# Kernel tuning notes

Measured on AMD Instinct MI355X. Metric: run time of the kernel, lower is better.

Reference implementation:

```python
import jax, jax.numpy as jnp
import numpy as np

B = 262144
STATE_DIM = 12
ACTION_DIM = 1
MSG_DIM = 32
MAX_CHILDREN = 2
EPS = 1e-12  # F.normalize default eps


def _l2norm(x):
    n = jnp.sqrt(jnp.sum(x * x, axis=-1, keepdims=True))
    return x / jnp.maximum(n, EPS)


def setup_inputs() -> dict:
    key = jax.random.key(0)
    ks = jax.random.split(key, 16)

    def lin(kw, kb, out_d, in_d):
        lim = 1.0 / np.sqrt(in_d)
        w = jax.random.uniform(kw, (out_d, in_d), jnp.float32, -lim, lim)
        b = jax.random.uniform(kb, (out_d,), jnp.float32, -lim, lim)
        return w, b

    state = jax.random.normal(ks[0], (B, STATE_DIM), jnp.float32)
    action = jax.random.normal(ks[1], (B, ACTION_DIM), jnp.float32)

    # ModelUp (sNet): fc1, fc2, fc3
    up_w1, up_b1 = lin(ks[2], ks[3], 64, STATE_DIM + ACTION_DIM)
    up_w2, up_b2 = lin(ks[4], ks[5], 64, 64 + MSG_DIM * MAX_CHILDREN)
    up_w3, up_b3 = lin(ks[6], ks[7], MSG_DIM, 64)

    # ModelDownAction.model = MLPBase(msg_dim + action_dim + msg_dim, msg_dim)
    dyn_w1, dyn_b1 = lin(ks[8], ks[9], 400, MSG_DIM + ACTION_DIM + MSG_DIM)
    dyn_w2, dyn_b2 = lin(ks[10], ks[11], 300, 400)
    dyn_w3, dyn_b3 = lin(ks[12], ks[13], MSG_DIM, 300)

    return dict(state=state, action=action,
                up_w1=up_w1, up_b1=up_b1, up_w2=up_w2, up_b2=up_b2,
                up_w3=up_w3, up_b3=up_b3,
                dyn_w1=dyn_w1, dyn_b1=dyn_b1, dyn_w2=dyn_w2, dyn_b2=dyn_b2,
                dyn_w3=dyn_w3, dyn_b3=dyn_b3)


def reference(state, action,
              up_w1, up_b1, up_w2, up_b2, up_w3, up_b3,
              dyn_w1, dyn_b1, dyn_w2, dyn_b2, dyn_w3, dyn_b3):
    # num_limbs == 1, parents = [-1], td = bu = True, disable_fold = True
    x = state                              # (B, state_dim)
    u = action                             # (B, 1)

    # ---- bottom_up_transmission(0): ModelUp with all-zero child messages ----
    m_children = jnp.zeros((B, MSG_DIM * MAX_CHILDREN), x.dtype)
    xu = jnp.concatenate([x, u], axis=-1)
    xu = _l2norm(xu @ up_w1.T + up_b1)                       # (B, 64)
    xum = jnp.tanh(jnp.concatenate([xu, m_children], axis=-1))
    xum = jnp.tanh(xum @ up_w2.T + up_b2)                    # (B, 64)
    msg_up = _l2norm(xum @ up_w3.T + up_b3)                  # (B, msg_dim)

    # ---- top_down_transmission(0): ModelDownAction, state := msg_up ----
    # parent_msg = zeros, self_children_idx = 0 -> msg_in = zeros slice
    msg_in = jnp.zeros((B, MSG_DIM), x.dtype)
    xum2 = jnp.concatenate([msg_up, u, msg_in], axis=-1)     # (B, 2*msg_dim+1)
    h = jax.nn.relu(xum2 @ dyn_w1.T + dyn_b1)                # (B, 400)
    h = jax.nn.relu(h @ dyn_w2.T + dyn_b2)                   # (B, 300)
    delta = h @ dyn_w3.T + dyn_b3                            # (B, msg_dim)

    # stack over num_limbs=1 then squeeze -> (B, msg_dim)
    return delta
```

## Files before the change

### kernel.cpp

```cpp
#include <hip/hip_runtime.h>
#include <stdint.h>

typedef short s16x8 __attribute__((ext_vector_type(8)));
typedef float f32x16 __attribute__((ext_vector_type(16)));
typedef unsigned int u32;
typedef unsigned int u32x2 __attribute__((ext_vector_type(2)));

#define NFRAG 336
#define WS_USHORTS (NFRAG*512)
#define PANEL_BYTES 16384
#define LDS_BYTES (2*PANEL_BYTES)

#define MFMA(a,b,c) __builtin_amdgcn_mfma_f32_32x32x16_bf16((a),(b),(c),0,0,0)

__device__ __forceinline__ unsigned short f2bf(float f){
  u32 x = __builtin_bit_cast(u32, f);
  x += 0x7fffu + ((x >> 16) & 1u);
  return (unsigned short)(x >> 16);
}

__device__ __forceinline__ float bfhi(float b){
  return __builtin_bit_cast(float, (u32)f2bf(b) << 16);
}

__device__ __forceinline__ u32 pkbf(float a, float b){
  u32 r;
  asm("v_cvt_pk_bf16_f32 %0, %1, %2" : "=v"(r) : "v"(a), "v"(b));
  return r;
}

__device__ __forceinline__ float fast_tanh(float x){
  float ax = fabsf(x);
  float e = __expf(-2.0f * ax);
  float r = (1.0f - e) * __builtin_amdgcn_rcpf(1.0f + e);
  return x < 0.0f ? -r : r;
}

__device__ __forceinline__ float halfsum(float s){
  return s + __shfl_xor(s, 32);
}

__device__ __forceinline__ void tile2frags(const f32x16 v, s16x8& f0, s16x8& f1){
  u32 w00 = pkbf(v[0],  v[1]),  w01 = pkbf(v[2],  v[3]);
  u32 w10 = pkbf(v[4],  v[5]),  w11 = pkbf(v[6],  v[7]);
  u32 w20 = pkbf(v[8],  v[9]),  w21 = pkbf(v[10], v[11]);
  u32 w30 = pkbf(v[12], v[13]), w31 = pkbf(v[14], v[15]);
  u32x2 p0 = __builtin_amdgcn_permlane32_swap(w00, w10, false, false);
  u32x2 p1 = __builtin_amdgcn_permlane32_swap(w01, w11, false, false);
  u32x2 p2 = __builtin_amdgcn_permlane32_swap(w20, w30, false, false);
  u32x2 p3 = __builtin_amdgcn_permlane32_swap(w21, w31, false, false);
  int4 r0, r1;
  r0.x = (int)p0[0]; r0.y = (int)p1[0]; r0.z = (int)p0[1]; r0.w = (int)p1[1];
  r1.x = (int)p2[0]; r1.y = (int)p3[0]; r1.z = (int)p2[1]; r1.w = (int)p3[1];
  f0 = __builtin_bit_cast(s16x8, r0);
  f1 = __builtin_bit_cast(s16x8, r1);
}

__global__ void wconv_kernel(const float* __restrict__ uw1, const float* __restrict__ ub1,
                             const float* __restrict__ uw2, const float* __restrict__ ub2,
                             const float* __restrict__ uw3, const float* __restrict__ ub3,
                             const float* __restrict__ dw1, const float* __restrict__ db1,
                             const float* __restrict__ dw2, const float* __restrict__ db2,
                             const float* __restrict__ dw3, const float* __restrict__ db3,
                             unsigned short* __restrict__ wp)
{
  int i = blockIdx.x*256 + threadIdx.x;
  if (i >= WS_USHORTS) return;
  int f    = i >> 9;
  int lane = (i >> 3) & 63;
  int j    = i & 7;
  int row  = lane & 31;
  int k8   = (lane >> 5)*8 + j;
  float v = 0.0f;
  if (f < 2){
    int feat = f*32 + row; int k = k8;
    if (k < 13) v = uw1[feat*13 + k];
    else if (k == 13) v = ub1[feat];
    else if (k == 14) v = ub1[feat] - bfhi(ub1[feat]);
  } else if (f < 12){
    int t = f - 2; int kt = t >> 1, nt = t & 1;
    int feat = nt*32 + row; int k = kt*16 + k8;
    if (k < 64) v = uw2[feat*128 + k];
    else if (k == 64) v = ub2[feat];
    else if (k == 65) v = ub2[feat] - bfhi(ub2[feat]);
  } else if (f < 17){
    int kt = f - 12; int feat = row; int k = kt*16 + k8;
    if (k < 64) v = uw3[feat*64 + k];
    else if (k == 64) v = ub3[feat];
    else if (k == 65) v = ub3[feat] - bfhi(ub3[feat]);
  } else if (f < 56){
    int t = f - 17; int nt = t/3, kt = t%3;
    int feat = nt*32 + row; int k = kt*16 + k8;
    if (feat < 400){
      if (k < 33) v = dw1[feat*65 + k];
      else if (k == 33) v = db1[feat];
      else if (k == 34) v = db1[feat] - bfhi(db1[feat]);
    } else if ((feat == 400 || feat == 401) && k == 33) v = 1.0f;
  } else {
    int t = f - 56; int n = t/56; int r = t%56;
    if (r < 52){
      int kf = r >> 1, nt = r & 1;
      int feat = n*64 + nt*32 + row; int k = kf*16 + k8;
      if (feat < 300){
        if (k < 400) v = dw2[feat*400 + k];
        else if (k == 400) v = db2[feat];
        else if (k == 401) v = db2[feat] - bfhi(db2[feat]);
      } else if ((feat == 300 || feat == 301) && k == 400) v = 1.0f;
    } else {
      int kt = n*4 + (r - 52); int feat = row; int k = kt*16 + k8;
      if (k < 300) v = dw3[feat*300 + k];
      else if (k == 300) v = db3[feat];
      else if (k == 301) v = db3[feat] - bfhi(db3[feat]);
    }
  }
  wp[i] = f2bf(v);
}

__device__ __forceinline__ s16x8 fragF(const char* sm, int f, int ln){
  return *(const s16x8*)(sm + ((f >> 4) & 1)*PANEL_BYTES + (f & 15)*1024 + ln*16);
}

__device__ __forceinline__ void stage16(const unsigned short* wp, char* sm, int panel, int tid){
  char* dst = sm + (panel & 1)*PANEL_BYTES;
  const char* src = (const char*)wp + (size_t)panel*PANEL_BYTES;
  #pragma unroll
  for (int j = 0; j < 8; ++j){
    int off = j*2048 + tid*16;
    __builtin_amdgcn_global_load_lds(
      (const __attribute__((address_space(1))) unsigned int*)(src + off),
      (__attribute__((address_space(3))) unsigned int*)(dst + off), 16, 0, 0);
  }
}

#define BND(P) { __syncthreads(); if ((P) <= 20) stage16(wp, sm, (P), tid); }

#define D1TRIPLE(f0_, oA, oB) { \
  f32x16 a = {}; \
  __builtin_amdgcn_s_setprio(1); \
  a = MFMA(fragF(sm, (f0_)+0, ln), mf0, a); \
  a = MFMA(fragF(sm, (f0_)+1, ln), mf1, a); \
  a = MFMA(fragF(sm, (f0_)+2, ln), mf2, a); \
  __builtin_amdgcn_s_setprio(0); \
  _Pragma("unroll") \
  for (int r = 0; r < 16; ++r) a[r] = fmaxf(a[r], 0.f); \
  tile2frags(a, oA, oB); }

#define D2RUN(fb, r0, r1) { \
  __builtin_amdgcn_s_setprio(1); \
  _Pragma("unroll") \
  for (int r = (r0); r < (r1); ++r){ \
    s16x8 hb = h1f[r>>1]; \
    if (r & 1) d2a1 = MFMA(fragF(sm, (fb)+r, ln), hb, d2a1); \
    else       d2a0 = MFMA(fragF(sm, (fb)+r, ln), hb, d2a0); \
  } \
  __builtin_amdgcn_s_setprio(0); }

#define D2TAIL(fb) { \
  _Pragma("unroll") \
  for (int r = 0; r < 16; ++r){ \
    d2a0[r] = fmaxf(d2a0[r], 0.f); \
    d2a1[r] = fmaxf(d2a1[r], 0.f); \
  } \
  s16x8 c0, c1, c2, c3; \
  tile2frags(d2a0, c0, c1); \
  tile2frags(d2a1, c2, c3); \
  __builtin_amdgcn_s_setprio(1); \
  acc3 = MFMA(fragF(sm, (fb)+52, ln), c0, acc3); \
  acc3 = MFMA(fragF(sm, (fb)+53, ln), c1, acc3); \
  acc3 = MFMA(fragF(sm, (fb)+54, ln), c2, acc3); \
  acc3 = MFMA(fragF(sm, (fb)+55, ln), c3, acc3); \
  __builtin_amdgcn_s_setprio(0); }

__global__ __launch_bounds__(128, 2) void fused_kernel(
    const float* __restrict__ state, const float* __restrict__ action,
    const unsigned short* __restrict__ wp, float* __restrict__ out)
{
  __shared__ __align__(1024) char sm[LDS_BYTES];

  const int tid = threadIdx.x;
  const int ln  = tid & 63;
  const int wid = tid >> 6;
  const int c   = ln & 31;
  const int h   = ln >> 5;
  const int rowb = blockIdx.x*64 + wid*32;

  const float* xr = state + (size_t)(rowb + c)*12;
  float u = action[rowb + c];
  float4 xa, xb;
  if (h == 0){
    xa = *(const float4*)xr;
    xb = *(const float4*)(xr + 4);
  } else {
    xa = *(const float4*)(xr + 8);
    xb = float4{u, 1.0f, 1.0f, 0.0f};
  }

  stage16(wp, sm, 0, tid);
  BND(1)

  int4 xw;
  xw.x = pkbf(xa.x, xa.y); xw.y = pkbf(xa.z, xa.w);
  xw.z = pkbf(xb.x, xb.y); xw.w = pkbf(xb.z, xb.w);
  s16x8 xfrag = __builtin_bit_cast(s16x8, xw);
  int4 ow = {0,0,0,0}; if (h == 0) ow.x = 0x3F803F80;
  s16x8 onef = __builtin_bit_cast(s16x8, ow);
  int4 mw = {0,0,0,0};
  if (h == 0){ mw.x = pkbf(u, 1.0f); mw.y = 0x3F80; }
  s16x8 mf2 = __builtin_bit_cast(s16x8, mw);

  s16x8 mf0, mf1;
  {
    s16x8 xf0, xf1, xf2, xf3, tf0, tf1, tf2, tf3;
    {
      f32x16 a0 = {}, a1 = {};
      a0 = MFMA(fragF(sm, 0, ln), xfrag, a0);
      a1 = MFMA(fragF(sm, 1, ln), xfrag, a1);
      float s = 0.f;
      #pragma unroll
      for (int r = 0; r < 16; ++r) s += a0[r]*a0[r] + a1[r]*a1[r];
      s = halfsum(s);
      float inv = __builtin_amdgcn_rsqf(fmaxf(s, 1e-24f));
      #pragma unroll
      for (int r = 0; r < 16; ++r){
        a0[r] = fast_tanh(a0[r]*inv);
        a1[r] = fast_tanh(a1[r]*inv);
      }
      tile2frags(a0, xf0, xf1);
      tile2frags(a1, xf2, xf3);
    }
    {
      f32x16 a0 = {}, a1 = {};
      __builtin_amdgcn_s_setprio(1);
      a0 = MFMA(fragF(sm, 2, ln), xf0, a0);  a1 = MFMA(fragF(sm, 3, ln), xf0, a1);
      a0 = MFMA(fragF(sm, 4, ln), xf1, a0);  a1 = MFMA(fragF(sm, 5, ln), xf1, a1);
      a0 = MFMA(fragF(sm, 6, ln), xf2, a0);  a1 = MFMA(fragF(sm, 7, ln), xf2, a1);
      a0 = MFMA(fragF(sm, 8, ln), xf3, a0);  a1 = MFMA(fragF(sm, 9, ln), xf3, a1);
      a0 = MFMA(fragF(sm,10, ln), onef, a0); a1 = MFMA(fragF(sm,11, ln), onef, a1);
      __builtin_amdgcn_s_setprio(0);
      #pragma unroll
      for (int r = 0; r < 16; ++r){
        a0[r] = fast_tanh(a0[r]);
        a1[r] = fast_tanh(a1[r]);
      }
      tile2frags(a0, tf0, tf1);
      tile2frags(a1, tf2, tf3);
    }
    {
      f32x16 m = {};
      __builtin_amdgcn_s_setprio(1);
      m = MFMA(fragF(sm,12, ln), tf0, m);
      m = MFMA(fragF(sm,13, ln), tf1, m);
      m = MFMA(fragF(sm,14, ln), tf2, m);
      m = MFMA(fragF(sm,15, ln), tf3, m);
      __builtin_amdgcn_s_setprio(0);
      BND(2)
      __builtin_amdgcn_s_setprio(1);
      m = MFMA(fragF(sm,16, ln), onef, m);
      __builtin_amdgcn_s_setprio(0);
      float s = 0.f;
      #pragma unroll
      for (int r = 0; r < 16; ++r) s += m[r]*m[r];
      s = halfsum(s);
      float inv = __builtin_amdgcn_rsqf(fmaxf(s, 1e-24f));
      #pragma unroll
      for (int r = 0; r < 16; ++r) m[r] *= inv;
      tile2frags(m, mf0, mf1);
    }
  }

  s16x8 h1f[26];
  D1TRIPLE(17, h1f[0],  h1f[1])
  D1TRIPLE(20, h1f[2],  h1f[3])
  D1TRIPLE(23, h1f[4],  h1f[5])
  D1TRIPLE(26, h1f[6],  h1f[7])
  D1TRIPLE(29, h1f[8],  h1f[9])
  BND(3)
  D1TRIPLE(32, h1f[10], h1f[11])
  D1TRIPLE(35, h1f[12], h1f[13])
  D1TRIPLE(38, h1f[14], h1f[15])
  D1TRIPLE(41, h1f[16], h1f[17])
  D1TRIPLE(44, h1f[18], h1f[19])
  {
    f32x16 a = {};
    __builtin_amdgcn_s_setprio(1);
    a = MFMA(fragF(sm, 47, ln), mf0, a);
    __builtin_amdgcn_s_setprio(0);
    BND(4)
    __builtin_amdgcn_s_setprio(1);
    a = MFMA(fragF(sm, 48, ln), mf1, a);
    a = MFMA(fragF(sm, 49, ln), mf2, a);
    __builtin_amdgcn_s_setprio(0);
    #pragma unroll
    for (int r = 0; r < 16; ++r) a[r] = fmaxf(a[r], 0.f);
    tile2frags(a, h1f[20], h1f[21]);
  }
  D1TRIPLE(50, h1f[22], h1f[23])
  D1TRIPLE(53, h1f[24], h1f[25])

  f32x16 acc3 = {};
  {
    f32x16 d2a0 = {}, d2a1 = {};
    D2RUN(56, 0, 8)
    BND(5)
    D2RUN(56, 8, 24)
    BND(6)
    D2RUN(56, 24, 40)
    BND(7)
    D2RUN(56, 40, 52)
    D2TAIL(56)
  }
  {
    f32x16 d2a0 = {}, d2a1 = {};
    BND(8)
    D2RUN(112, 0, 16)
    BND(9)
    D2RUN(112, 16, 32)
    BND(10)
    D2RUN(112, 32, 48)
    BND(11)
    D2RUN(112, 48, 52)
    D2TAIL(112)
  }
  {
    f32x16 d2a0 = {}, d2a1 = {};
    D2RUN(168, 0, 8)
    BND(12)
    D2RUN(168, 8, 24)
    BND(13)
    D2RUN(168, 24, 40)
    BND(14)
    D2RUN(168, 40, 52)
    D2TAIL(168)
  }
  {
    f32x16 d2a0 = {}, d2a1 = {};
    BND(15)
    D2RUN(224, 0, 16)
    BND(16)
    D2RUN(224, 16, 32)
    BND(17)
    D2RUN(224, 32, 48)
    BND(18)
    D2RUN(224, 48, 52)
    D2TAIL(224)
  }
  {
    f32x16 d2a0 = {}, d2a1 = {};
    D2RUN(280, 0, 8)
    BND(19)
    D2RUN(280, 8, 24)
    BND(20)
    D2RUN(280, 24, 40)
    BND(21)
    D2RUN(280, 40, 52)
    D2TAIL(280)
  }

  float* op = out + (size_t)(rowb + c)*32;
  #pragma unroll
  for (int p = 0; p < 4; ++p){
    float4 v4 = {acc3[4*p+0], acc3[4*p+1], acc3[4*p+2], acc3[4*p+3]};
    *(float4*)(op + p*8 + h*4) = v4;
  }
}

extern "C" void kernel_launch(void* const* d_in, const int* in_sizes, int n_in,
                              void* d_out, int out_size, void* d_ws, size_t ws_size,
                              hipStream_t stream)
{
  const float* state  = (const float*)d_in[0];
  const float* action = (const float*)d_in[1];
  const float* up_w1  = (const float*)d_in[2];
  const float* up_b1  = (const float*)d_in[3];
  const float* up_w2  = (const float*)d_in[4];
  const float* up_b2  = (const float*)d_in[5];
  const float* up_w3  = (const float*)d_in[6];
  const float* up_b3  = (const float*)d_in[7];
  const float* dyn_w1 = (const float*)d_in[8];
  const float* dyn_b1 = (const float*)d_in[9];
  const float* dyn_w2 = (const float*)d_in[10];
  const float* dyn_b2 = (const float*)d_in[11];
  const float* dyn_w3 = (const float*)d_in[12];
  const float* dyn_b3 = (const float*)d_in[13];
  unsigned short* wp = (unsigned short*)d_ws;

  hipLaunchKernelGGL(wconv_kernel, dim3((WS_USHORTS + 255)/256), dim3(256), 0, stream,
                     up_w1, up_b1, up_w2, up_b2, up_w3, up_b3,
                     dyn_w1, dyn_b1, dyn_w2, dyn_b2, dyn_w3, dyn_b3, wp);
  hipLaunchKernelGGL(fused_kernel, dim3(262144/64), dim3(128), 0, stream,
                     state, action, wp, (float*)d_out);
}
```

Measured before the change: 104.6 us.

## Use 4-wave blocks with 24-fragment weight panels to amortize LDS staging

Blocks grow from 2 to 4 waves (128 rows each), so every weight panel staged into LDS serves twice as many rows and global weight traffic per row halves. Panels grow from 16 to 24 fragments (24 KB, 48 KB double-buffered), which cuts the number of barriers and staging points from 21 to 14. The barrier placement is reworked to match the new panel boundaries. The cost is that each barrier now waits on 4 waves, and LDS per block is larger, which may limit how many blocks fit per CU.

```diff
diff --git a/kernel.cpp b/kernel.cpp
--- a/kernel.cpp
+++ b/kernel.cpp
@@ -8,7 +8,8 @@
 
 #define NFRAG 336
 #define WS_USHORTS (NFRAG*512)
-#define PANEL_BYTES 16384
+#define PANEL_FRAGS 24
+#define PANEL_BYTES (PANEL_FRAGS*1024)
 #define LDS_BYTES (2*PANEL_BYTES)
 
 #define MFMA(a,b,c) __builtin_amdgcn_mfma_f32_32x32x16_bf16((a),(b),(c),0,0,0)
@@ -117,22 +118,23 @@
 }
 
 __device__ __forceinline__ s16x8 fragF(const char* sm, int f, int ln){
-  return *(const s16x8*)(sm + ((f >> 4) & 1)*PANEL_BYTES + (f & 15)*1024 + ln*16);
-}
-
-__device__ __forceinline__ void stage16(const unsigned short* wp, char* sm, int panel, int tid){
+  return *(const s16x8*)(sm + ((f/PANEL_FRAGS) & 1)*PANEL_BYTES
+                            + (f % PANEL_FRAGS)*1024 + ln*16);
+}
+
+__device__ __forceinline__ void stage24(const unsigned short* wp, char* sm, int panel, int tid){
   char* dst = sm + (panel & 1)*PANEL_BYTES;
   const char* src = (const char*)wp + (size_t)panel*PANEL_BYTES;
   #pragma unroll
-  for (int j = 0; j < 8; ++j){
-    int off = j*2048 + tid*16;
+  for (int j = 0; j < 6; ++j){
+    int off = j*4096 + tid*16;
     __builtin_amdgcn_global_load_lds(
       (const __attribute__((address_space(1))) unsigned int*)(src + off),
       (__attribute__((address_space(3))) unsigned int*)(dst + off), 16, 0, 0);
   }
 }
 
-#define BND(P) { __syncthreads(); if ((P) <= 20) stage16(wp, sm, (P), tid); }
+#define BND(NP) { __syncthreads(); if ((NP) <= 13) stage24(wp, sm, (NP), tid); }
 
 #define D1TRIPLE(f0_, oA, oB) { \
   f32x16 a = {}; \
@@ -171,7 +173,7 @@
   acc3 = MFMA(fragF(sm, (fb)+55, ln), c3, acc3); \
   __builtin_amdgcn_s_setprio(0); }
 
-__global__ __launch_bounds__(128, 2) void fused_kernel(
+__global__ __launch_bounds__(256, 2) void fused_kernel(
     const float* __restrict__ state, const float* __restrict__ action,
     const unsigned short* __restrict__ wp, float* __restrict__ out)
 {
@@ -182,7 +184,7 @@
   const int wid = tid >> 6;
   const int c   = ln & 31;
   const int h   = ln >> 5;
-  const int rowb = blockIdx.x*64 + wid*32;
+  const int rowb = blockIdx.x*128 + wid*32;
 
   const float* xr = state + (size_t)(rowb + c)*12;
   float u = action[rowb + c];
@@ -195,8 +197,9 @@
     xb = float4{u, 1.0f, 1.0f, 0.0f};
   }
 
-  stage16(wp, sm, 0, tid);
-  BND(1)
+  stage24(wp, sm, 0, tid);
+  __syncthreads();
+  stage24(wp, sm, 1, tid);
 
   int4 xw;
   xw.x = pkbf(xa.x, xa.y); xw.y = pkbf(xa.z, xa.w);
@@ -252,9 +255,6 @@
       m = MFMA(fragF(sm,13, ln), tf1, m);
       m = MFMA(fragF(sm,14, ln), tf2, m);
       m = MFMA(fragF(sm,15, ln), tf3, m);
-      __builtin_amdgcn_s_setprio(0);
-      BND(2)
-      __builtin_amdgcn_s_setprio(1);
       m = MFMA(fragF(sm,16, ln), onef, m);
       __builtin_amdgcn_s_setprio(0);
       float s = 0.f;
@@ -271,10 +271,22 @@
   s16x8 h1f[26];
   D1TRIPLE(17, h1f[0],  h1f[1])
   D1TRIPLE(20, h1f[2],  h1f[3])
-  D1TRIPLE(23, h1f[4],  h1f[5])
+  {
+    f32x16 a = {};
+    __builtin_amdgcn_s_setprio(1);
+    a = MFMA(fragF(sm, 23, ln), mf0, a);
+    __builtin_amdgcn_s_setprio(0);
+    BND(2)
+    __builtin_amdgcn_s_setprio(1);
+    a = MFMA(fragF(sm, 24, ln), mf1, a);
+    a = MFMA(fragF(sm, 25, ln), mf2, a);
+    __builtin_amdgcn_s_setprio(0);
+    #pragma unroll
+    for (int r = 0; r < 16; ++r) a[r] = fmaxf(a[r], 0.f);
+    tile2frags(a, h1f[4], h1f[5]);
+  }
   D1TRIPLE(26, h1f[6],  h1f[7])
   D1TRIPLE(29, h1f[8],  h1f[9])
-  BND(3)
   D1TRIPLE(32, h1f[10], h1f[11])
   D1TRIPLE(35, h1f[12], h1f[13])
   D1TRIPLE(38, h1f[14], h1f[15])
@@ -285,7 +297,7 @@
     __builtin_amdgcn_s_setprio(1);
     a = MFMA(fragF(sm, 47, ln), mf0, a);
     __builtin_amdgcn_s_setprio(0);
-    BND(4)
+    BND(3)
     __builtin_amdgcn_s_setprio(1);
     a = MFMA(fragF(sm, 48, ln), mf1, a);
     a = MFMA(fragF(sm, 49, ln), mf2, a);
@@ -300,59 +312,48 @@
   f32x16 acc3 = {};
   {
     f32x16 d2a0 = {}, d2a1 = {};
-    D2RUN(56, 0, 8)
+    D2RUN(56, 0, 16)
+    BND(4)
+    D2RUN(56, 16, 40)
     BND(5)
-    D2RUN(56, 8, 24)
-    BND(6)
-    D2RUN(56, 24, 40)
-    BND(7)
     D2RUN(56, 40, 52)
     D2TAIL(56)
   }
   {
     f32x16 d2a0 = {}, d2a1 = {};
+    D2RUN(112, 0, 8)
+    BND(6)
+    D2RUN(112, 8, 32)
+    BND(7)
+    D2RUN(112, 32, 52)
+    D2TAIL(112)
+  }
+  {
+    f32x16 d2a0 = {}, d2a1 = {};
     BND(8)
-    D2RUN(112, 0, 16)
+    D2RUN(168, 0, 24)
     BND(9)
-    D2RUN(112, 16, 32)
+    D2RUN(168, 24, 48)
     BND(10)
-    D2RUN(112, 32, 48)
+    D2RUN(168, 48, 52)
+    D2TAIL(168)
+  }
+  {
+    f32x16 d2a0 = {}, d2a1 = {};
+    D2RUN(224, 0, 16)
     BND(11)
-    D2RUN(112, 48, 52)
-    D2TAIL(112)
-  }
-  {
-    f32x16 d2a0 = {}, d2a1 = {};
-    D2RUN(168, 0, 8)
+    D2RUN(224, 16, 40)
     BND(12)
-    D2RUN(168, 8, 24)
+    D2RUN(224, 40, 52)
+    D2TAIL(224)
+  }
+  {
+    f32x16 d2a0 = {}, d2a1 = {};
+    D2RUN(280, 0, 8)
     BND(13)
-    D2RUN(168, 24, 40)
+    D2RUN(280, 8, 32)
     BND(14)
-    D2RUN(168, 40, 52)
-    D2TAIL(168)
-  }
-  {
-    f32x16 d2a0 = {}, d2a1 = {};
-    BND(15)
-    D2RUN(224, 0, 16)
-    BND(16)
-    D2RUN(224, 16, 32)
-    BND(17)
-    D2RUN(224, 32, 48)
-    BND(18)
-    D2RUN(224, 48, 52)
-    D2TAIL(224)
-  }
-  {
-    f32x16 d2a0 = {}, d2a1 = {};
-    D2RUN(280, 0, 8)
-    BND(19)
-    D2RUN(280, 8, 24)
-    BND(20)
-    D2RUN(280, 24, 40)
-    BND(21)
-    D2RUN(280, 40, 52)
+    D2RUN(280, 32, 52)
     D2TAIL(280)
   }
 
@@ -387,6 +388,6 @@
   hipLaunchKernelGGL(wconv_kernel, dim3((WS_USHORTS + 255)/256), dim3(256), 0, stream,
                      up_w1, up_b1, up_w2, up_b2, up_w3, up_b3,
                      dyn_w1, dyn_b1, dyn_w2, dyn_b2, dyn_w3, dyn_b3, wp);
-  hipLaunchKernelGGL(fused_kernel, dim3(262144/64), dim3(128), 0, stream,
+  hipLaunchKernelGGL(fused_kernel, dim3(262144/128), dim3(256), 0, stream,
                      state, action, wp, (float*)d_out);
 }
```

Result: faster. 93.63 us (-10.5%).
